# Kernel optimization log

Hardware: AMD Instinct MI355X
Metric: run time of the kernel (lower is better)

## Reference

```python
import jax, jax.numpy as jnp
import numpy as np
import math

N, LQ, C, HD, L, P = 2, 17821, 256, 8, 4, 4
D = C // HD
SHAPES = [(100, 134), (50, 67), (25, 34), (13, 17)]


def setup_inputs() -> dict:
    key = jax.random.key(0)
    ks = jax.random.split(key, 8)
    shapes = np.array(SHAPES, np.int32)
    areas = shapes[:, 0] * shapes[:, 1]
    starts = np.concatenate([[0], np.cumsum(areas)[:-1]]).astype(np.int32)
    Lin = int(areas.sum())
    sc = 1.0 / math.sqrt(C)
    # sampling_offsets bias: radial grid init as in _reset_parameters
    thetas = np.arange(HD, dtype=np.float32) * (2.0 * math.pi / HD)
    grid = np.stack([np.cos(thetas), np.sin(thetas)], -1)
    grid = grid / np.abs(grid).max(-1, keepdims=True)
    grid = np.tile(grid[:, None, None, :], (1, L, P, 1)) * np.arange(1, P + 1, dtype=np.float32)[None, None, :, None]
    boff = jnp.asarray(grid.reshape(-1), jnp.float32)
    return dict(
        query=jax.random.normal(ks[0], (N, LQ, C), jnp.float32),
        reference_points=jax.random.uniform(ks[1], (N, LQ, L, 2), jnp.float32),
        input_flatten=jax.random.normal(ks[2], (N, Lin, C), jnp.float32),
        input_spatial_shapes=jnp.asarray(shapes),
        input_level_start_index=jnp.asarray(starts),
        Wv=jax.random.normal(ks[3], (C, C), jnp.float32) * sc,
        bv=jnp.zeros((C,), jnp.float32),
        Woff=jax.random.normal(ks[4], (C, HD * L * P * 2), jnp.float32) * 0.01,
        boff=boff,
        Watt=jax.random.normal(ks[5], (C, HD * L * P), jnp.float32) * 0.02,
        batt=jnp.zeros((HD * L * P,), jnp.float32),
        Wout=jax.random.normal(ks[6], (C, C), jnp.float32) * sc,
        bout=jnp.zeros((C,), jnp.float32),
    )


def _ms_deform_attn_core(value, shapes, starts, loc, attw):
    # value: (N, Len_in, HD, D); loc: (N, Lq, HD, L, P, 2) in [0,1]; attw: (N, Lq, HD, L, P)
    n, lq = loc.shape[0], loc.shape[1]
    out = jnp.zeros((n, lq, HD, D), value.dtype)
    for l in range(L):
        H, W = int(shapes[l, 0]), int(shapes[l, 1])
        s = int(starts[l])
        v = value[:, s:s + H * W]                                    # (N, HW, HD, D)
        # (N,Lq,HD,P,2) -> (N,Lq,P,HD,2) -> (N,Lq*P,HD) per coord
        locl = loc[:, :, :, l].transpose(0, 1, 3, 2, 4).reshape(n, lq * P, HD, 2)
        # grid_sample align_corners=False mapping
        x = locl[..., 0] * W - 0.5
        y = locl[..., 1] * H - 0.5
        x0f, y0f = jnp.floor(x), jnp.floor(y)
        fx, fy = x - x0f, y - y0f
        x0, y0 = x0f.astype(jnp.int32), y0f.astype(jnp.int32)

        def corner(xi, yi, w):
            valid = (xi >= 0) & (xi < W) & (yi >= 0) & (yi < H)      # zero padding
            idx = jnp.clip(yi, 0, H - 1) * W + jnp.clip(xi, 0, W - 1)
            g = jnp.take_along_axis(v, idx[..., None], axis=1)        # (N, Lq*P, HD, D)
            return g * (w * valid)[..., None]

        samp = (corner(x0, y0, (1 - fx) * (1 - fy))
                + corner(x0 + 1, y0, fx * (1 - fy))
                + corner(x0, y0 + 1, (1 - fx) * fy)
                + corner(x0 + 1, y0 + 1, fx * fy))                    # (N, Lq*P, HD, D)
        aw = attw[:, :, :, l].transpose(0, 1, 3, 2).reshape(n, lq * P, HD)
        out = out + (samp * aw[..., None]).reshape(n, lq, P, HD, D).sum(axis=2)
    return out.reshape(n, lq, HD * D)


def reference(query, reference_points, input_flatten, input_spatial_shapes,
              input_level_start_index, Wv, bv, Woff, boff, Watt, batt, Wout, bout):
    shapes = np.asarray(input_spatial_shapes)
    starts = np.asarray(input_level_start_index)
    n, lq, _ = query.shape
    value = (input_flatten @ Wv + bv).reshape(n, -1, HD, D)
    offsets = (query @ Woff + boff).reshape(n, lq, HD, L, P, 2)
    # reference_points has last dim 2 -> normalize offsets by (W, H) per level
    norm = jnp.asarray(shapes[:, ::-1], jnp.float32)                  # (L, 2) = (W, H)
    loc = reference_points[:, :, None, :, None, :] + offsets / norm[None, None, None, :, None, :]
    attw = (query @ Watt + batt).reshape(n, lq, HD, L * P)
    attw = jax.nn.softmax(attw, axis=-1).reshape(n, lq, HD, L, P)
    out = _ms_deform_attn_core(value, shapes, starts, loc, attw)
    return out @ Wout + bout
```

## Files before the change

kernel.cpp:

```cpp
#include <hip/hip_runtime.h>
#include <hip/hip_bf16.h>
#include <math.h>

#define NB    2
#define LQ    17821
#define LIN   17821
#define CCH   256
#define HDN   8
#define DCH   32
#define LVL   4
#define NPT   4
#define KDIM  256

__constant__ const int   cH[LVL]  = {100, 50, 25, 13};
__constant__ const int   cW[LVL]  = {134, 67, 34, 17};
__constant__ const int   cS[LVL]  = {0, 13400, 16750, 17600};
__constant__ const float cHf[LVL] = {100.f, 50.f, 25.f, 13.f};
__constant__ const float cWf[LVL] = {134.f, 67.f, 34.f, 17.f};
__constant__ const float cRH[LVL] = {1.f/100.f, 1.f/50.f, 1.f/25.f, 1.f/13.f};
__constant__ const float cRW[LVL] = {1.f/134.f, 1.f/67.f, 1.f/34.f, 1.f/17.f};

typedef __attribute__((ext_vector_type(8))) _Float16 f16x8;
typedef __attribute__((ext_vector_type(4))) _Float16 f16x4;
typedef __attribute__((ext_vector_type(4))) float    f32x4;

__device__ __forceinline__ void glds16(const void* g, void* l) {
    __builtin_amdgcn_global_load_lds(
        (const __attribute__((address_space(1))) void*)g,
        (__attribute__((address_space(3))) void*)l, 16, 0, 0);
}

__global__ void prep_all(const float* __restrict__ Wv,
                         const float* __restrict__ Woff,
                         const float* __restrict__ Watt,
                         const float* __restrict__ Wout,
                         const float* __restrict__ boff,
                         const float* __restrict__ batt,
                         _Float16* __restrict__ wvT,
                         _Float16* __restrict__ wqT,
                         _Float16* __restrict__ wuT,
                         float* __restrict__ b384)
{
    const int i = blockIdx.x * 256 + threadIdx.x;
    if (i < 65536) {
        const int n = i >> 8, k = i & 255;
        wvT[i] = (_Float16)Wv[(size_t)k * 256 + n];
    } else if (i < 131072) {
        const int j = i - 65536, n = j >> 8, k = j & 255;
        wqT[j] = (_Float16)Woff[(size_t)k * 256 + n];
    } else if (i < 163840) {
        const int j = i - 131072, n = j >> 8, k = j & 255;
        wqT[65536 + j] = (_Float16)Watt[(size_t)k * 128 + n];
    } else if (i < 229376) {
        const int j = i - 163840, n = j >> 8, k = j & 255;
        wuT[j] = (_Float16)Wout[(size_t)k * 256 + n];
    } else {
        const int j = i - 229376;
        if (j < 256)      b384[j] = boff[j];
        else if (j < 384) b384[j] = batt[j - 256];
    }
}

template<typename AT, typename OutT, bool PERM>
__global__ __launch_bounds__(256, 2) void gemm_tile(
    const AT* __restrict__ A,
    const _Float16* __restrict__ BT,
    const float* __restrict__ bias, OutT* __restrict__ C,
    int M, int Ntot)
{
    __shared__ _Float16 As[2][4096];
    __shared__ _Float16 Bs[2][4096];

    const int t    = threadIdx.x;
    const int wav  = t >> 6;
    const int lane = t & 63;
    const int bm   = blockIdx.y * 128;
    const int bn   = blockIdx.x * 128;

    const int wr = wav >> 1, wc = wav & 1;
    const int fcol = lane & 15;
    const int fk   = lane >> 4;

    int aoff[4], boff[4];
#pragma unroll
    for (int i = 0; i < 4; ++i) {
        const int ar = wr * 64 + i * 16 + fcol;
        aoff[i] = ar * 64 + ((fk ^ ((ar >> 1) & 3)) << 4);
        const int br = wc * 64 + i * 16 + fcol;
        boff[i] = br * 64 + ((fk ^ ((br >> 1) & 3)) << 4);
    }

    const int srow = lane >> 2;
    const int slot = lane & 3;

    f32x4 acc[4][4];
#pragma unroll
    for (int i = 0; i < 4; ++i)
#pragma unroll
        for (int j = 0; j < 4; ++j) acc[i][j] = (f32x4)(0.f);

    auto stage = [&](int s, int buf) {
#pragma unroll
        for (int i = 0; i < 2; ++i) {
            const int j   = wav + i * 4;
            const int row = j * 16 + srow;
            const int swz = ((row >> 1) & 3) << 4;
            const int rga = min(bm + row, M - 1);
            if constexpr (sizeof(AT) == 2) {
                const int kb = (slot << 4) ^ swz;
                glds16((const char*)A + (size_t)rga * 512 + s * 64 + kb,
                       (char*)As[buf] + j * 1024);
            } else {
                const char* src = (const char*)A + (size_t)rga * 1024 + s * 128 + slot * 32;
                const float4 u0 = *reinterpret_cast<const float4*>(src);
                const float4 u1 = *reinterpret_cast<const float4*>(src + 16);
                f16x8 hv;
                hv[0] = (_Float16)u0.x; hv[1] = (_Float16)u0.y;
                hv[2] = (_Float16)u0.z; hv[3] = (_Float16)u0.w;
                hv[4] = (_Float16)u1.x; hv[5] = (_Float16)u1.y;
                hv[6] = (_Float16)u1.z; hv[7] = (_Float16)u1.w;
                *reinterpret_cast<f16x8*>((char*)As[buf] + j * 1024 + srow * 64
                                          + ((slot << 4) ^ swz)) = hv;
            }
            {
                const int kb = (slot << 4) ^ swz;
                const int rgb = bn + row;
                glds16((const char*)BT + (size_t)rgb * 512 + s * 64 + kb,
                       (char*)Bs[buf] + j * 1024);
            }
        }
    };

    stage(0, 0);
    __syncthreads();
    int cur = 0;
#pragma unroll 1
    for (int s = 0; s < 8; ++s) {
        if (s + 1 < 8) stage(s + 1, cur ^ 1);
        f16x8 af[4], bfr[4];
#pragma unroll
        for (int i = 0; i < 4; ++i) {
            af[i]  = *reinterpret_cast<const f16x8*>((const char*)As[cur] + aoff[i]);
            bfr[i] = *reinterpret_cast<const f16x8*>((const char*)Bs[cur] + boff[i]);
        }
#pragma unroll
        for (int mi = 0; mi < 4; ++mi)
#pragma unroll
            for (int ni = 0; ni < 4; ++ni)
                acc[mi][ni] = __builtin_amdgcn_mfma_f32_16x16x32_f16(
                    af[mi], bfr[ni], acc[mi][ni], 0, 0, 0);
        __syncthreads();
        cur ^= 1;
    }

    const int r0 = bm + wr * 64 + (lane >> 4) * 4;
    const int c0 = bn + wc * 64 + fcol;
#pragma unroll
    for (int ni = 0; ni < 4; ++ni) {
        const int col = c0 + ni * 16;
        const float bv = bias[col];
#pragma unroll
        for (int mi = 0; mi < 4; ++mi) {
#pragma unroll
            for (int j = 0; j < 4; ++j) {
                const int r = r0 + mi * 16 + j;
                if (r < M) {
                    const float v = acc[mi][ni][j] + bv;
                    if (PERM) {
                        const int n   = (r >= LIN) ? 1 : 0;
                        const int pos = r - n * LIN;
                        const size_t dst = ((size_t)(n * HDN + (col >> 5)) * LIN + pos) * 32 + (col & 31);
                        C[dst] = (OutT)v;
                    } else {
                        C[(size_t)r * Ntot + col] = (OutT)v;
                    }
                }
            }
        }
    }
}

__global__ __launch_bounds__(256) void msda_sample(
    const _Float16* __restrict__ value,
    const _Float16* __restrict__ qproj,
    const float* __restrict__ refp,
    _Float16* __restrict__ o16)
{
    __shared__ int2 sIW[2][HDN][16][4];

    const int t = threadIdx.x;

    {
        const int qs = t >> 7;
        const int h  = (t >> 4) & 7;
        const int ip = t & 15;
        const int l  = ip >> 2;

        const int r = blockIdx.x * 2 + qs;
        const int n = r / LQ;
        const _Float16* qrow = qproj + (size_t)r * 384;

        const float logit = (float)qrow[256 + h * 16 + ip];
        float m = logit;
#pragma unroll
        for (int k = 8; k >= 1; k >>= 1) m = fmaxf(m, __shfl_xor(m, k));
        const float e = __expf(logit - m);
        float s = e;
#pragma unroll
        for (int k = 8; k >= 1; k >>= 1) s += __shfl_xor(s, k);
        const float aw = e / s;

        const float ox = (float)qrow[h * 32 + ip * 2 + 0];
        const float oy = (float)qrow[h * 32 + ip * 2 + 1];
        const float rx = refp[(size_t)r * 8 + l * 2 + 0];
        const float ry = refp[(size_t)r * 8 + l * 2 + 1];

        const int   Ww = cW[l], Hh = cH[l], st = cS[l];
        const float Wf = cWf[l], Hf = cHf[l];
        const float rW = cRW[l], rH = cRH[l];

        const float x = (rx + ox * rW) * Wf - 0.5f;
        const float y = (ry + oy * rH) * Hf - 0.5f;
        const float x0f = floorf(x);
        const float y0f = floorf(y);
        const float fx = x - x0f;
        const float fy = y - y0f;
        const int x0 = (int)x0f, y0 = (int)y0f;
        const int x1 = x0 + 1,   y1 = y0 + 1;

        const bool vx0 = (x0 >= 0) & (x0 < Ww);
        const bool vx1 = (x1 >= 0) & (x1 < Ww);
        const bool vy0 = (y0 >= 0) & (y0 < Hh);
        const bool vy1 = (y1 >= 0) & (y1 < Hh);

        const float gx0 = 1.f - fx, gx1 = fx;
        const float gy0 = 1.f - fy, gy1 = fy;

        const float w00 = (vx0 & vy0) ? gx0 * gy0 * aw : 0.f;
        const float w10 = (vx1 & vy0) ? gx1 * gy0 * aw : 0.f;
        const float w01 = (vx0 & vy1) ? gx0 * gy1 * aw : 0.f;
        const float w11 = (vx1 & vy1) ? gx1 * gy1 * aw : 0.f;

        const int xc0 = min(max(x0, 0), Ww - 1);
        const int xc1 = min(max(x1, 0), Ww - 1);
        const int yc0 = min(max(y0, 0), Hh - 1);
        const int yc1 = min(max(y1, 0), Hh - 1);

        const int base = (n * HDN + h) * LIN + st;
        sIW[qs][h][ip][0] = make_int2((base + yc0 * Ww + xc0) * 64, __float_as_int(w00));
        sIW[qs][h][ip][1] = make_int2((base + yc0 * Ww + xc1) * 64, __float_as_int(w10));
        sIW[qs][h][ip][2] = make_int2((base + yc1 * Ww + xc0) * 64, __float_as_int(w01));
        sIW[qs][h][ip][3] = make_int2((base + yc1 * Ww + xc1) * 64, __float_as_int(w11));
    }

    __syncthreads();

    const int g   = t >> 5;
    const int w   = t & 31;
    const int sub = w & 3;
    const int lv  = (w >> 2) & 3;
    const int q   = w >> 4;
    const char* vbase = (const char*)value + sub * 16;

    int2 iw[4][4];
#pragma unroll
    for (int i = 0; i < 4; ++i)
#pragma unroll
        for (int c = 0; c < 4; ++c)
            iw[i][c] = sIW[q][g][lv * 4 + i][c];

    f16x8 v[4][4];
#pragma unroll
    for (int i = 0; i < 4; ++i)
#pragma unroll
        for (int c = 0; c < 4; ++c)
            v[i][c] = *reinterpret_cast<const f16x8*>(vbase + iw[i][c].x);

    __builtin_amdgcn_sched_barrier(0);

    float acc[8] = {};
#pragma unroll
    for (int i = 0; i < 4; ++i) {
#pragma unroll
        for (int c = 0; c < 4; ++c) {
            const float wt = __int_as_float(iw[i][c].y);
#pragma unroll
            for (int j = 0; j < 8; ++j)
                acc[j] = fmaf((float)v[i][c][j], wt, acc[j]);
        }
    }

#pragma unroll
    for (int k = 4; k <= 8; k <<= 1)
#pragma unroll
        for (int j = 0; j < 8; ++j)
            acc[j] += __shfl_xor(acc[j], k);

    if ((w & 12) == 0) {
        const int r = blockIdx.x * 2 + q;
        const size_t o = (size_t)r * 256 + g * 32 + sub * 8;
        f16x8 hv;
#pragma unroll
        for (int j = 0; j < 8; ++j) hv[j] = (_Float16)acc[j];
        *reinterpret_cast<f16x8*>(&o16[o]) = hv;
    }
}

extern "C" void kernel_launch(void* const* d_in, const int* in_sizes, int n_in,
                              void* d_out, int out_size, void* d_ws, size_t ws_size,
                              hipStream_t stream)
{
    const float* query  = (const float*)d_in[0];
    const float* refp   = (const float*)d_in[1];
    const float* inflat = (const float*)d_in[2];
    const float* Wv     = (const float*)d_in[5];
    const float* bv     = (const float*)d_in[6];
    const float* Woff   = (const float*)d_in[7];
    const float* boff   = (const float*)d_in[8];
    const float* Watt   = (const float*)d_in[9];
    const float* batt   = (const float*)d_in[10];
    const float* Wout   = (const float*)d_in[11];
    const float* bout   = (const float*)d_in[12];
    float* out = (float*)d_out;

    const int M = NB * LQ;
    const size_t MC = (size_t)M * 256;

    float* ws   = (float*)d_ws;
    float* b384 = ws;

    _Float16* fbase = (_Float16*)(b384 + 384);
    _Float16* qp16  = fbase;
    _Float16* v16   = qp16 + (size_t)M * 384;
    _Float16* o16   = v16 + MC;
    _Float16* wvT   = o16 + MC;
    _Float16* wqT   = wvT + 65536;
    _Float16* wuT   = wqT + 98304;

    const dim3 blk(256);
    const int mblk = (M + 127) / 128;

    prep_all<<<dim3(898), blk, 0, stream>>>(Wv, Woff, Watt, Wout, boff, batt,
                                            wvT, wqT, wuT, b384);

    gemm_tile<float, _Float16, true><<<dim3(2, mblk), blk, 0, stream>>>(inflat, wvT, bv, v16, M, 256);
    gemm_tile<float, _Float16, false><<<dim3(3, mblk), blk, 0, stream>>>(query, wqT, b384, qp16, M, 384);

    msda_sample<<<dim3(M / 2), blk, 0, stream>>>(v16, qp16, refp, o16);

    gemm_tile<_Float16, float, false><<<dim3(2, mblk), blk, 0, stream>>>(o16, wuT, bout, out, M, 256);
}
```

Measured before the change: 167.8 us.

## Remap sampling blocks to one head and a chunk of 16 queries

Each sampling block now handles one (batch, head) pair across 16 consecutive queries instead of all 8 heads for 2 queries. Blocks are ordered so neighbouring blocks touch the same head's value plane. The aim is better L2/cache locality for the value gathers, and the shared-memory index table is padded (stride 81/5) to cut LDS bank conflicts. In exchange, the query-projection row reads become strided across heads, and the last chunk does duplicated work through clamped rows.

After: 159.6 us. 1.05x faster.

```diff
diff --git a/kernel.cpp b/kernel.cpp
--- a/kernel.cpp
+++ b/kernel.cpp
@@ -11,6 +11,8 @@
 #define LVL   4
 #define NPT   4
 #define KDIM  256
+#define QCH   16
+#define NCHUNK ((LQ + QCH - 1) / QCH)
 
 __constant__ const int   cH[LVL]  = {100, 50, 25, 13};
 __constant__ const int   cW[LVL]  = {134, 67, 34, 17};
@@ -186,19 +188,23 @@
     const float* __restrict__ refp,
     _Float16* __restrict__ o16)
 {
-    __shared__ int2 sIW[2][HDN][16][4];
-
-    const int t = threadIdx.x;
+    __shared__ int2 sIW[QCH * 81 + 4];
+
+    const int t   = threadIdx.x;
+    const int bid = blockIdx.x;
+    const int chunk = bid % NCHUNK;
+    const int nh    = bid / NCHUNK;
+    const int h     = nh & 7;
+    const int n     = nh >> 3;
 
     {
-        const int qs = t >> 7;
-        const int h  = (t >> 4) & 7;
+        const int q1 = t >> 4;
         const int ip = t & 15;
         const int l  = ip >> 2;
 
-        const int r = blockIdx.x * 2 + qs;
-        const int n = r / LQ;
-        const _Float16* qrow = qproj + (size_t)r * 384;
+        const int rq  = min(chunk * QCH + q1, LQ - 1);
+        const int row = n * LQ + rq;
+        const _Float16* qrow = qproj + (size_t)row * 384;
 
         const float logit = (float)qrow[256 + h * 16 + ip];
         float m = logit;
@@ -212,8 +218,8 @@
 
         const float ox = (float)qrow[h * 32 + ip * 2 + 0];
         const float oy = (float)qrow[h * 32 + ip * 2 + 1];
-        const float rx = refp[(size_t)r * 8 + l * 2 + 0];
-        const float ry = refp[(size_t)r * 8 + l * 2 + 1];
+        const float rx = refp[(size_t)row * 8 + l * 2 + 0];
+        const float ry = refp[(size_t)row * 8 + l * 2 + 1];
 
         const int   Ww = cW[l], Hh = cH[l], st = cS[l];
         const float Wf = cWf[l], Hf = cHf[l];
@@ -246,20 +252,19 @@
         const int yc0 = min(max(y0, 0), Hh - 1);
         const int yc1 = min(max(y1, 0), Hh - 1);
 
-        const int base = (n * HDN + h) * LIN + st;
-        sIW[qs][h][ip][0] = make_int2((base + yc0 * Ww + xc0) * 64, __float_as_int(w00));
-        sIW[qs][h][ip][1] = make_int2((base + yc0 * Ww + xc1) * 64, __float_as_int(w10));
-        sIW[qs][h][ip][2] = make_int2((base + yc1 * Ww + xc0) * 64, __float_as_int(w01));
-        sIW[qs][h][ip][3] = make_int2((base + yc1 * Ww + xc1) * 64, __float_as_int(w11));
+        const int base = (nh * LIN + st) * 64;
+        const int b0   = q1 * 81 + ip * 5;
+        sIW[b0 + 0] = make_int2(base + (yc0 * Ww + xc0) * 64, __float_as_int(w00));
+        sIW[b0 + 1] = make_int2(base + (yc0 * Ww + xc1) * 64, __float_as_int(w10));
+        sIW[b0 + 2] = make_int2(base + (yc1 * Ww + xc0) * 64, __float_as_int(w01));
+        sIW[b0 + 3] = make_int2(base + (yc1 * Ww + xc1) * 64, __float_as_int(w11));
     }
 
     __syncthreads();
 
-    const int g   = t >> 5;
-    const int w   = t & 31;
-    const int sub = w & 3;
-    const int lv  = (w >> 2) & 3;
-    const int q   = w >> 4;
+    const int q1  = t >> 4;
+    const int lv  = (t >> 2) & 3;
+    const int sub = t & 3;
     const char* vbase = (const char*)value + sub * 16;
 
     int2 iw[4][4];
@@ -267,7 +272,7 @@
     for (int i = 0; i < 4; ++i)
 #pragma unroll
         for (int c = 0; c < 4; ++c)
-            iw[i][c] = sIW[q][g][lv * 4 + i][c];
+            iw[i][c] = sIW[q1 * 81 + (lv * 4 + i) * 5 + c];
 
     f16x8 v[4][4];
 #pragma unroll
@@ -296,9 +301,10 @@
         for (int j = 0; j < 8; ++j)
             acc[j] += __shfl_xor(acc[j], k);
 
-    if ((w & 12) == 0) {
-        const int r = blockIdx.x * 2 + q;
-        const size_t o = (size_t)r * 256 + g * 32 + sub * 8;
+    if ((t & 12) == 0) {
+        const int rq  = min(chunk * QCH + q1, LQ - 1);
+        const int row = n * LQ + rq;
+        const size_t o = (size_t)row * 256 + h * 32 + sub * 8;
         f16x8 hv;
 #pragma unroll
         for (int j = 0; j < 8; ++j) hv[j] = (_Float16)acc[j];
@@ -346,7 +352,7 @@
     gemm_tile<float, _Float16, true><<<dim3(2, mblk), blk, 0, stream>>>(inflat, wvT, bv, v16, M, 256);
     gemm_tile<float, _Float16, false><<<dim3(3, mblk), blk, 0, stream>>>(query, wqT, b384, qp16, M, 384);
 
-    msda_sample<<<dim3(M / 2), blk, 0, stream>>>(v16, qp16, refp, o16);
+    msda_sample<<<dim3(NB * HDN * NCHUNK), blk, 0, stream>>>(v16, qp16, refp, o16);
 
     gemm_tile<_Float16, float, false><<<dim3(2, mblk), blk, 0, stream>>>(o16, wuT, bout, out, M, 256);
 }
```
